# Kernel tuning notes

Measured on AMD Instinct MI355X. Metric: run time of the kernel, lower is better.

The kernel has to match this reference:

```python
import jax, jax.numpy as jnp
import numpy as np

B, S, D = 4, 4096, 64   # batch, seq_len, input_size
H, HD = 4, 16           # num_heads, head_dim


def setup_inputs() -> dict:
    key = jax.random.key(0)
    ks = jax.random.split(key, 9)
    sd = 1.0 / np.sqrt(D)          # torch Linear default uniform(-1/sqrt(fan_in), ...)
    so = 1.0 / np.sqrt(H * HD)
    u = lambda k, shape, s: jax.random.uniform(k, shape, jnp.float32, -s, s)
    return {
        "x": jax.random.normal(ks[0], (B, S, D), jnp.float32),
        "Wq": u(ks[1], (H, D, HD), sd), "bq": u(ks[2], (H, HD), sd),
        "Wk": u(ks[3], (H, D, HD), sd), "bk": u(ks[4], (H, HD), sd),
        "Wv": u(ks[5], (H, D, HD), sd), "bv": u(ks[6], (H, HD), sd),
        "Wo": u(ks[7], (H * HD, D), so), "bo": u(ks[8], (D,), so),
    }


def reference(x, Wq, bq, Wk, bk, Wv, bv, Wo, bo):
    # Batched per-head projections (fuses the original per-head Linear loop)
    q = jnp.einsum('bsd,hde->bhse', x, Wq) + bq[None, :, None, :]
    k = jnp.einsum('bsd,hde->bhse', x, Wk) + bk[None, :, None, :]
    v = jnp.einsum('bsd,hde->bhse', x, Wv) + bv[None, :, None, :]
    # scores: [B, H, S(query), S(key)]
    scores = jnp.einsum('bhse,bhte->bhst', q, k) / np.sqrt(HD).astype(np.float32)
    # FAITHFUL quirk: torch Softmax(dim=1) on [B,S,S] normalizes over the QUERY axis
    w = jax.nn.softmax(scores, axis=2)
    attended = jnp.einsum('bhst,bhte->bhse', w, v)          # [B,H,S,HD]
    concat = attended.transpose(0, 2, 1, 3).reshape(B, S, H * HD)
    out = concat @ Wo + bo                                   # [B,S,D]
    # FAITHFUL quirk: final softmax over the sequence axis (dim=1)
    return jax.nn.softmax(out, axis=1)
```

## Files before the change

kernel.cpp:

```cpp
#include <hip/hip_runtime.h>
#include <hip/hip_bf16.h>


#define BB 4
#define SS 4096
#define DD 64
#define HH 4
#define HDD 16

typedef unsigned int u32;
typedef unsigned short u16;
typedef __attribute__((ext_vector_type(8))) short bfrag;
typedef __attribute__((ext_vector_type(4))) float floatx4;
typedef __attribute__((ext_vector_type(16))) float floatx16;
typedef __attribute__((ext_vector_type(2))) u32 u32x2;
typedef __attribute__((ext_vector_type(4))) u32 u32x4;

#define LOG2E 1.4426950408889634074f
#define QSCALE (LOG2E * 0.25f)

__device__ __forceinline__ float fexp2(float x) {
#if __has_builtin(__builtin_amdgcn_exp2f)
  return __builtin_amdgcn_exp2f(x);
#else
  float r; asm("v_exp_f32 %0, %1" : "=v"(r) : "v"(x)); return r;
#endif
}
__device__ __forceinline__ float frcp(float x) {
#if __has_builtin(__builtin_amdgcn_rcpf)
  return __builtin_amdgcn_rcpf(x);
#else
  float r; asm("v_rcp_f32 %0, %1" : "=v"(r) : "v"(x)); return r;
#endif
}

__device__ __forceinline__ u16 f2bf(float f) {
  u32 u = __builtin_bit_cast(u32, f);
  return (u16)((u + 0x7FFFu + ((u >> 16) & 1u)) >> 16);
}
__device__ __forceinline__ u32 pack_bf(float lo, float hi) {
#if __has_builtin(__builtin_amdgcn_perm)
  return __builtin_amdgcn_perm(__builtin_bit_cast(u32, hi),
                               __builtin_bit_cast(u32, lo), 0x07060302u);
#else
  u32 a = __builtin_bit_cast(u32, lo);
  u32 b = __builtin_bit_cast(u32, hi);
  return (a >> 16) | (b & 0xFFFF0000u);
#endif
}

__device__ __forceinline__ void gload_lds16(const u16* g, u16* l) {
  __builtin_amdgcn_global_load_lds(
      (const __attribute__((address_space(1))) void*)(g),
      (__attribute__((address_space(3))) void*)(l), 16, 0, 0);
}

__device__ __forceinline__ int tmap(int c) {
  int c5 = c & 31;
  return (c & ~31) + (c5 & 3) + ((c5 >> 2) & 1) * 8 + ((c5 >> 3) & 1) * 16
       + ((c5 >> 4) & 1) * 4;
}

__global__ __launch_bounds__(256) void k_proj(
    const float* __restrict__ x,
    const float* __restrict__ Wq, const float* __restrict__ bq,
    const float* __restrict__ Wk, const float* __restrict__ bk,
    const float* __restrict__ Wv, const float* __restrict__ bv,
    u16* __restrict__ qb, u16* __restrict__ kfl, float* __restrict__ vf)
{
  __shared__ float xs[16 * 64];
  const int tid = threadIdx.x;
  const int blk = blockIdx.x;
  const int b   = blk >> 8;
  const int s0  = (blk & 255) << 4;
  ((float4*)xs)[tid] = ((const float4*)(x + ((size_t)b * SS + s0) * DD))[tid];
  __syncthreads();

  const int col = tid & 63, h = col >> 4, e = col & 15;
  const int rg  = tid >> 6;
  float aq[4] = {0,0,0,0}, ak[4] = {0,0,0,0}, av[4] = {0,0,0,0};
  const int wofs = h * (DD * HDD) + e;
#pragma unroll 4
  for (int d = 0; d < DD; ++d) {
    float wq = Wq[wofs + d * HDD];
    float wk = Wk[wofs + d * HDD];
    float wv = Wv[wofs + d * HDD];
    const float* xr = xs + (rg * 4) * 64 + d;
#pragma unroll
    for (int r = 0; r < 4; ++r) {
      float xv = xr[r * 64];
      aq[r] += xv * wq; ak[r] += xv * wk; av[r] += xv * wv;
    }
  }
  const float bqv = bq[col], bkv = bk[col], bvv = bv[col];
  const int bh = b * HH + h;
  size_t base = ((size_t)bh * SS + (s0 + rg * 4)) * HDD + e;
#pragma unroll
  for (int r = 0; r < 4; ++r) {
    int t = s0 + rg * 4 + r;
    qb[base + r * HDD] = f2bf((aq[r] + bqv) * QSCALE);
    vf[base + r * HDD] = av[r] + bvv;
    size_t kidx = (((size_t)bh * 128 + (t >> 5)) * 64
                 + (e >> 3) * 32 + (t & 31)) * 8 + (e & 7);
    kfl[kidx] = f2bf(ak[r] + bkv);
  }
}

__global__ __launch_bounds__(512, 4) void k_csvp(
    const u16* __restrict__ qb, const u16* __restrict__ kfl,
    const float* __restrict__ vf, u16* __restrict__ vp)
{
  __shared__ float vstage[128 * 16];
  __shared__ float cpart[2][128];
  __shared__ float rcl[128];
  const int tid = threadIdx.x;
  const int lane = tid & 63, w = tid >> 6;
  const int l31 = lane & 31, hl = lane >> 5;
  const int bx = blockIdx.x;
  const int bh = blockIdx.y;
  const int shalf = w >> 2;
  const size_t base = (size_t)bh * (SS * HDD);

  {
    const float4* vsrc4 = (const float4*)(vf + ((size_t)bh * SS + bx * 128) * HDD);
    ((float4*)vstage)[tid] = vsrc4[tid];
  }

  const int g = bx * 4 + (w & 3);
  const bfrag kf = *(const bfrag*)(kfl + (((size_t)bh * 128 + g) * 64 + lane) * 8);
  const u16* qpc = qb + base + ((size_t)shalf * 2048 + l31) * HDD + hl * 8;
  const floatx16 z16 = {0.f};
  float c0 = 0.f, c1 = 0.f, c2 = 0.f, c3 = 0.f;

#define LQ(i) (*(const bfrag*)(qpc + (size_t)(i) * (32 * HDD)))
#define ACCUM(dv)                                   \
  do {                                              \
    _Pragma("unroll")                               \
    for (int j = 0; j < 4; ++j) {                   \
      c0 += fexp2((dv)[4 * j + 0]);                 \
      c1 += fexp2((dv)[4 * j + 1]);                 \
      c2 += fexp2((dv)[4 * j + 2]);                 \
      c3 += fexp2((dv)[4 * j + 3]);                 \
    }                                               \
  } while (0)
#define STEP(qr, ri)                                                        \
  do {                                                                      \
    floatx16 dB = __builtin_amdgcn_mfma_f32_32x32x16_bf16(qr, kf, z16, 0, 0, 0); \
    qr = LQ(ri);                                                            \
    ACCUM(dA);                                                              \
    dA = dB;                                                                \
  } while (0)

  bfrag q0 = LQ(0), q1 = LQ(1), q2v = LQ(2), q3 = LQ(3);
  floatx16 dA = __builtin_amdgcn_mfma_f32_32x32x16_bf16(q0, kf, z16, 0, 0, 0);
  q0 = LQ(4);
#pragma unroll 1
  for (int o = 0; o < 2; ++o) {
#pragma unroll
    for (int i = 0; i < 32; i += 4) {
      STEP(q1,  i + 5);
      STEP(q2v, i + 6);
      STEP(q3,  i + 7);
      STEP(q0,  i + 8);
    }
    qpc += 32 * 32 * HDD;
  }
#undef STEP
#undef LQ
#undef ACCUM

  float c = (c0 + c1) + (c2 + c3);
  c += __shfl_xor(c, 32, 64);
  if (hl == 0)
    cpart[shalf][(w & 3) * 32 + l31] = c;
  __syncthreads();
  if (tid < 128)
    rcl[tid] = frcp(cpart[0][tid] + cpart[1][tid]);
  __syncthreads();

  if (tid < 256) {
    const int e = tid >> 4;
    const int h0 = bx & 1;
    const int poff = h0 * 16 + (tid & 15);
    const int cc = poff ^ (e & 7);
    const int h128 = h0 * 128;
    u32 r[4];
#pragma unroll
    for (int jj = 0; jj < 4; ++jj) {
      int ta = tmap(cc * 8 + 2 * jj)     - h128;
      int tb = tmap(cc * 8 + 2 * jj + 1) - h128;
      u16 lo = f2bf(vstage[ta * 16 + e] * rcl[ta]);
      u16 hi = f2bf(vstage[tb * 16 + e] * rcl[tb]);
      r[jj] = (u32)lo | ((u32)hi << 16);
    }
    u16* outb = vp + ((size_t)bh * 16 + (bx >> 1)) * 4096;
    u32x4 vv = {r[0], r[1], r[2], r[3]};
    *(u32x4*)(outb + e * 256 + poff * 8) = vv;
  }
}

__global__ __launch_bounds__(256, 4) void k_attn(
    const u16* __restrict__ qb, const u16* __restrict__ kfl,
    const u16* __restrict__ vp, float* __restrict__ attp)
{
  __shared__ __align__(16) u16 vls[2][4096];
  __shared__ __align__(16) u16 kls[2][4096];
  const int tid  = threadIdx.x;
  const int lane = tid & 63, w = tid >> 6;
  const int l31 = lane & 31, hl = lane >> 5;
  const int bh = blockIdx.z, b = bh >> 2, h = bh & 3;
  const int tph = blockIdx.y;
  const int s0 = blockIdx.x * 128 + w * 32;
  const size_t base = (size_t)bh * (SS * HDD);

  const bfrag qf = *(const bfrag*)(qb + base + (size_t)(s0 + l31) * HDD + hl * 8);
  const floatx16 z16 = {0.f};
  floatx16 acc0 = {0.f}, acc1 = {0.f};

  const u16* vsrc = vp  + ((size_t)bh * 16  + tph * 8)  * 4096;
  const u16* ksrc = kfl + ((size_t)bh * 128 + tph * 64) * 512;

#define STAGE(ch, buf)                                                \
  do {                                                                \
    const u16* gv = vsrc + (ch) * 4096 + w * 1024 + lane * 8;         \
    u16* lv = &vls[buf][0] + w * 1024;                                \
    gload_lds16(gv, lv);                                              \
    gload_lds16(gv + 512, lv + 512);                                  \
    const u16* gk = ksrc + (ch) * 4096 + w * 1024 + lane * 8;         \
    u16* lk = &kls[buf][0] + w * 1024;                                \
    gload_lds16(gk, lk);                                              \
    gload_lds16(gk + 512, lk + 512);                                  \
  } while (0)

  STAGE(0, 0);

#pragma unroll
  for (int ch = 0; ch < 8; ++ch) {
    asm volatile("s_waitcnt vmcnt(0)" ::: "memory");
    __builtin_amdgcn_s_barrier();
    __builtin_amdgcn_sched_barrier(0);
    if (ch < 7) STAGE(ch + 1, (ch + 1) & 1);

    const u16* vrow = &vls[ch & 1][0] + (l31 & 15) * 256;
    const u16* krow = &kls[ch & 1][0];
    const int eb = l31 & 7;

    bfrag kfr[4];
#pragma unroll
    for (int it = 0; it < 4; ++it)
      kfr[it] = *(const bfrag*)(krow + it * 512 + lane * 8);
    floatx16 dA = __builtin_amdgcn_mfma_f32_32x32x16_bf16(kfr[0], qf, z16, 0, 0, 0);

#pragma unroll
    for (int it = 0; it < 8; ++it) {
      if (it < 4)
        kfr[it & 3] = *(const bfrag*)(krow + (it + 4) * 512 + lane * 8);
      floatx16 dB;
      if (it < 7)
        dB = __builtin_amdgcn_mfma_f32_32x32x16_bf16(kfr[(it + 1) & 3], qf, z16, 0, 0, 0);
      else
        dB = dA;
      u32 wr[8];
#pragma unroll
      for (int p = 0; p < 8; ++p)
        wr[p] = pack_bf(fexp2(dA[2 * p]), fexp2(dA[2 * p + 1]));
      const int cc0 = it * 4 + hl * 2;
      u32x4 af0 = *(const u32x4*)(vrow + ((cc0 ^ eb) << 3));
      u32x4 af1 = *(const u32x4*)(vrow + (((cc0 + 1) ^ eb) << 3));
      u32x4 ef0 = {wr[0], wr[1], wr[2], wr[3]};
      u32x4 ef1 = {wr[4], wr[5], wr[6], wr[7]};
      acc0 = __builtin_amdgcn_mfma_f32_32x32x16_bf16(
          __builtin_bit_cast(bfrag, af0), __builtin_bit_cast(bfrag, ef0), acc0, 0, 0, 0);
      acc1 = __builtin_amdgcn_mfma_f32_32x32x16_bf16(
          __builtin_bit_cast(bfrag, af1), __builtin_bit_cast(bfrag, ef1), acc1, 0, 0, 0);
      dA = dB;
    }
  }
#undef STAGE

  floatx16 acc = acc0 + acc1;
  float* ao = attp + (((size_t)tph * BB + b) * SS + s0 + l31) * (HH * HDD)
            + h * HDD + 4 * hl;
  float4 lo4 = {acc[0], acc[1], acc[2], acc[3]};
  float4 hi4 = {acc[4], acc[5], acc[6], acc[7]};
  *(float4*)ao       = lo4;
  *(float4*)(ao + 8) = hi4;
}

__global__ __launch_bounds__(256) void k_oproj(
    const float* __restrict__ att, const float* __restrict__ Wo,
    const float* __restrict__ bo, float* __restrict__ outp,
    float* __restrict__ part)
{
  __shared__ float wols[64 * 64];
  __shared__ float atts[8][128];
  __shared__ float red[4][64];
  const int tid = threadIdx.x;
  const int blk = blockIdx.x;
  const int b = blk >> 9, s0 = (blk & 511) << 3;
#pragma unroll
  for (int i = 0; i < 4; ++i)
    ((float4*)wols)[tid + 256 * i] = ((const float4*)Wo)[tid + 256 * i];
  {
    const int r = tid >> 5, q = tid & 31;
    const int half = q >> 4, j4 = (q & 15) << 2;
    const float4 v = *(const float4*)(
        att + (((size_t)half * BB + b) * SS + s0 + r) * 64 + j4);
    *(float4*)(&atts[r][half * 64 + j4]) = v;
  }
  __syncthreads();

  const int d = tid & 63, sg = tid >> 6;
  const float bov = bo[d];
  float es = 0.f;
#pragma unroll
  for (int r = 0; r < 2; ++r) {
    const int row = sg * 2 + r;
    float acc = bov;
#pragma unroll
    for (int c = 0; c < 64; ++c)
      acc += (atts[row][c] + atts[row][64 + c]) * wols[c * 64 + d];
    outp[((size_t)b * SS + s0 + row) * 64 + d] = acc;
    es += fexp2(acc * LOG2E);
  }
  red[sg][d] = es;
  __syncthreads();
  if (tid < 64)
    part[((size_t)b * 512 + (blk & 511)) * 64 + tid] =
        red[0][tid] + red[1][tid] + red[2][tid] + red[3][tid];
}

__global__ __launch_bounds__(256) void k_softmax(
    const float* __restrict__ outp, const float* __restrict__ part,
    float* __restrict__ out)
{
  __shared__ float red[4][64];
  __shared__ float rs[64];
  const int tid = threadIdx.x, d = tid & 63, sg = tid >> 6;
  const int st = blockIdx.x;
  const int b = blockIdx.y;
  {
    float e = 0.f;
    const float* pp = part + ((size_t)b * 512 + sg * 128) * 64 + d;
#pragma unroll 8
    for (int c = 0; c < 128; ++c) e += pp[c * 64];
    red[sg][d] = e;
  }
  __syncthreads();
  if (tid < 64)
    rs[tid] = frcp(red[0][tid] + red[1][tid] + red[2][tid] + red[3][tid]);
  __syncthreads();
  const float r = rs[d];
  const size_t rowbase = ((size_t)b * SS + st * 64 + sg * 16) * 64 + d;
#pragma unroll 4
  for (int i = 0; i < 16; ++i)
    out[rowbase + i * 64] = fexp2(outp[rowbase + i * 64] * LOG2E) * r;
}

extern "C" void kernel_launch(void* const* d_in, const int* in_sizes, int n_in,
                              void* d_out, int out_size, void* d_ws, size_t ws_size,
                              hipStream_t stream) {
  const float* x  = (const float*)d_in[0];
  const float* Wq = (const float*)d_in[1];
  const float* bq = (const float*)d_in[2];
  const float* Wk = (const float*)d_in[3];
  const float* bk = (const float*)d_in[4];
  const float* Wv = (const float*)d_in[5];
  const float* bv = (const float*)d_in[6];
  const float* Wo = (const float*)d_in[7];
  const float* bo = (const float*)d_in[8];

  char* ws = (char*)d_ws;
  constexpr size_t QB_OFF  = 0;
  constexpr size_t KF_OFF  = (size_t)2  << 20;
  constexpr size_t VF_OFF  = (size_t)4  << 20;
  constexpr size_t VP_OFF  = (size_t)8  << 20;
  constexpr size_t ATT_OFF = (size_t)10 << 20;
  constexpr size_t OUT_OFF = (size_t)18 << 20;
  constexpr size_t PT_OFF  = (size_t)22 << 20;

  u16*   qb   = (u16*)  (ws + QB_OFF);
  u16*   kfl  = (u16*)  (ws + KF_OFF);
  float* vf   = (float*)(ws + VF_OFF);
  u16*   vpb  = (u16*)  (ws + VP_OFF);
  float* attp = (float*)(ws + ATT_OFF);
  float* outp = (float*)(ws + OUT_OFF);
  float* part = (float*)(ws + PT_OFF);
  float* out  = (float*)d_out;

  hipLaunchKernelGGL(k_proj,    dim3(1024),       dim3(256), 0, stream,
                     x, Wq, bq, Wk, bk, Wv, bv, qb, kfl, vf);
  hipLaunchKernelGGL(k_csvp,    dim3(32, 16),     dim3(512), 0, stream,
                     qb, kfl, vf, vpb);
  hipLaunchKernelGGL(k_attn,    dim3(32, 2, 16),  dim3(256), 0, stream,
                     qb, kfl, vpb, attp);
  hipLaunchKernelGGL(k_oproj,   dim3(2048),       dim3(256), 0, stream,
                     attp, Wo, bo, outp, part);
  hipLaunchKernelGGL(k_softmax, dim3(64, 4),      dim3(256), 0, stream, outp, part, out);
}
```

Measured before the change: 173.8 us.

## Software-pipeline attention loop: K frags from global, deferred PV MFMA, setprio

Drops K staging through LDS and loads K fragments straight from global memory into registers, prefetching the next chunk's fragments during the current one. The PV MFMAs are delayed by one iteration so the exp2/pack work overlaps the MFMAs, V fragments are prefetched one step ahead, and s_setprio raises priority around the MFMA issue. The vmcnt wait is relaxed and the outer loop is no longer unrolled, trading LDS traffic and barrier stalls for more register pressure and direct global loads.

```diff
diff --git a/kernel.cpp b/kernel.cpp
--- a/kernel.cpp
+++ b/kernel.cpp
@@ -204,7 +204,6 @@
     const u16* __restrict__ vp, float* __restrict__ attp)
 {
   __shared__ __align__(16) u16 vls[2][4096];
-  __shared__ __align__(16) u16 kls[2][4096];
   const int tid  = threadIdx.x;
   const int lane = tid & 63, w = tid >> 6;
   const int l31 = lane & 31, hl = lane >> 5;
@@ -219,6 +218,7 @@
 
   const u16* vsrc = vp  + ((size_t)bh * 16  + tph * 8)  * 4096;
   const u16* ksrc = kfl + ((size_t)bh * 128 + tph * 64) * 512;
+  const int eb = l31 & 7;
 
 #define STAGE(ch, buf)                                                \
   do {                                                                \
@@ -226,57 +226,80 @@
     u16* lv = &vls[buf][0] + w * 1024;                                \
     gload_lds16(gv, lv);                                              \
     gload_lds16(gv + 512, lv + 512);                                  \
-    const u16* gk = ksrc + (ch) * 4096 + w * 1024 + lane * 8;         \
-    u16* lk = &kls[buf][0] + w * 1024;                                \
-    gload_lds16(gk, lk);                                              \
-    gload_lds16(gk + 512, lk + 512);                                  \
   } while (0)
 
   STAGE(0, 0);
-
-#pragma unroll
+  bfrag kfr[4];
+#pragma unroll
+  for (int g = 0; g < 4; ++g)
+    kfr[g] = *(const bfrag*)(ksrc + (size_t)g * 512 + lane * 8);
+  floatx16 dA = __builtin_amdgcn_mfma_f32_32x32x16_bf16(kfr[0], qf, z16, 0, 0, 0);
+
+  u32x4 efL = {0,0,0,0}, efH = {0,0,0,0};
+  u32x4 afA0 = {0,0,0,0}, afA1 = {0,0,0,0};
+  u32x4 pf0, pf1;
+
+#pragma unroll 1
   for (int ch = 0; ch < 8; ++ch) {
-    asm volatile("s_waitcnt vmcnt(0)" ::: "memory");
+    asm volatile("s_waitcnt vmcnt(8)" ::: "memory");
     __builtin_amdgcn_s_barrier();
     __builtin_amdgcn_sched_barrier(0);
     if (ch < 7) STAGE(ch + 1, (ch + 1) & 1);
 
     const u16* vrow = &vls[ch & 1][0] + (l31 & 15) * 256;
-    const u16* krow = &kls[ch & 1][0];
-    const int eb = l31 & 7;
-
-    bfrag kfr[4];
-#pragma unroll
-    for (int it = 0; it < 4; ++it)
-      kfr[it] = *(const bfrag*)(krow + it * 512 + lane * 8);
-    floatx16 dA = __builtin_amdgcn_mfma_f32_32x32x16_bf16(kfr[0], qf, z16, 0, 0, 0);
+    {
+      const int cc = hl * 2;
+      pf0 = *(const u32x4*)(vrow + ((cc ^ eb) << 3));
+      pf1 = *(const u32x4*)(vrow + (((cc + 1) ^ eb) << 3));
+    }
 
 #pragma unroll
     for (int it = 0; it < 8; ++it) {
-      if (it < 4)
-        kfr[it & 3] = *(const bfrag*)(krow + (it + 4) * 512 + lane * 8);
+      __builtin_amdgcn_s_setprio(1);
       floatx16 dB;
       if (it < 7)
         dB = __builtin_amdgcn_mfma_f32_32x32x16_bf16(kfr[(it + 1) & 3], qf, z16, 0, 0, 0);
       else
-        dB = dA;
-      u32 wr[8];
-#pragma unroll
-      for (int p = 0; p < 8; ++p)
-        wr[p] = pack_bf(fexp2(dA[2 * p]), fexp2(dA[2 * p + 1]));
-      const int cc0 = it * 4 + hl * 2;
-      u32x4 af0 = *(const u32x4*)(vrow + ((cc0 ^ eb) << 3));
-      u32x4 af1 = *(const u32x4*)(vrow + (((cc0 + 1) ^ eb) << 3));
-      u32x4 ef0 = {wr[0], wr[1], wr[2], wr[3]};
-      u32x4 ef1 = {wr[4], wr[5], wr[6], wr[7]};
-      acc0 = __builtin_amdgcn_mfma_f32_32x32x16_bf16(
-          __builtin_bit_cast(bfrag, af0), __builtin_bit_cast(bfrag, ef0), acc0, 0, 0, 0);
-      acc1 = __builtin_amdgcn_mfma_f32_32x32x16_bf16(
-          __builtin_bit_cast(bfrag, af1), __builtin_bit_cast(bfrag, ef1), acc1, 0, 0, 0);
+        dB = __builtin_amdgcn_mfma_f32_32x32x16_bf16(kfr[0], qf, z16, 0, 0, 0);
+      if (it > 0 || ch > 0) {
+        acc0 = __builtin_amdgcn_mfma_f32_32x32x16_bf16(
+            __builtin_bit_cast(bfrag, afA0), __builtin_bit_cast(bfrag, efL), acc0, 0, 0, 0);
+        acc1 = __builtin_amdgcn_mfma_f32_32x32x16_bf16(
+            __builtin_bit_cast(bfrag, afA1), __builtin_bit_cast(bfrag, efH), acc1, 0, 0, 0);
+      }
+      __builtin_amdgcn_s_setprio(0);
+
+      if (it < 4)
+        kfr[it & 3] = *(const bfrag*)(ksrc + (size_t)(ch * 4096 + (it + 4) * 512) + lane * 8);
+      else if (ch < 7)
+        kfr[it & 3] = *(const bfrag*)(ksrc + (size_t)((ch + 1) * 4096 + (it - 4) * 512) + lane * 8);
+
+      afA0 = pf0; afA1 = pf1;
+      if (it < 7) {
+        const int cc = (it + 1) * 4 + hl * 2;
+        pf0 = *(const u32x4*)(vrow + ((cc ^ eb) << 3));
+        pf1 = *(const u32x4*)(vrow + (((cc + 1) ^ eb) << 3));
+      }
+
+      u32 w0 = pack_bf(fexp2(dA[0]),  fexp2(dA[1]));
+      u32 w1 = pack_bf(fexp2(dA[2]),  fexp2(dA[3]));
+      u32 w2 = pack_bf(fexp2(dA[4]),  fexp2(dA[5]));
+      u32 w3 = pack_bf(fexp2(dA[6]),  fexp2(dA[7]));
+      u32 w4 = pack_bf(fexp2(dA[8]),  fexp2(dA[9]));
+      u32 w5 = pack_bf(fexp2(dA[10]), fexp2(dA[11]));
+      u32 w6 = pack_bf(fexp2(dA[12]), fexp2(dA[13]));
+      u32 w7 = pack_bf(fexp2(dA[14]), fexp2(dA[15]));
+      efL = (u32x4){w0, w1, w2, w3};
+      efH = (u32x4){w4, w5, w6, w7};
       dA = dB;
     }
   }
 #undef STAGE
+
+  acc0 = __builtin_amdgcn_mfma_f32_32x32x16_bf16(
+      __builtin_bit_cast(bfrag, afA0), __builtin_bit_cast(bfrag, efL), acc0, 0, 0, 0);
+  acc1 = __builtin_amdgcn_mfma_f32_32x32x16_bf16(
+      __builtin_bit_cast(bfrag, afA1), __builtin_bit_cast(bfrag, efH), acc1, 0, 0, 0);
 
   floatx16 acc = acc0 + acc1;
   float* ao = attp + (((size_t)tph * BB + b) * SS + s0 + l31) * (HH * HDD)
```

After: 181.0 us. 4.2% more time.
